# Kernel optimization log

Hardware: AMD Instinct MI355X
Metric: run time of the kernel (lower is better)

Reference implementation:

```python
import jax, jax.numpy as jnp
import numpy as np
from jax import lax

B = 4096
PRO_VOCAB, PRO_LEN, PRO_K = 25, 1000, 8
LIG_VOCAB, LIG_LEN, LIG_K = 64, 100, 4
CH = 96  # 2*CH = 192 = 6*32 per the reshape in the original forward
DN = ('NCH', 'OIH', 'NCH')  # 1D conv dimension numbers


def setup_inputs() -> dict:
    key = jax.random.key(0)
    ks = jax.random.split(key, 8)
    protein = jax.random.normal(ks[0], (B, PRO_VOCAB, PRO_LEN), dtype=jnp.float32)
    ligand = jax.random.normal(ks[1], (B, LIG_VOCAB, LIG_LEN), dtype=jnp.float32)
    w_pro = jax.random.normal(ks[2], (CH, PRO_VOCAB, PRO_K), dtype=jnp.float32) * 0.05
    b_pro = jnp.zeros((CH,), dtype=jnp.float32)
    w_lig = jax.random.normal(ks[3], (CH, LIG_VOCAB, LIG_K), dtype=jnp.float32) * 0.05
    b_lig = jnp.zeros((CH,), dtype=jnp.float32)
    # QuLinear readout over the 32*32=1024 amplitude-encoded Gram matrix -> scalar
    w_aff = jax.random.normal(ks[4], (1024,), dtype=jnp.float32) * 0.05
    b_aff = jnp.zeros((), dtype=jnp.float32)
    return {"protein": protein, "ligand": ligand, "w_pro": w_pro, "b_pro": b_pro,
            "w_lig": w_lig, "b_lig": b_lig, "w_aff": w_aff, "b_aff": b_aff}


def _conv_branch(x, w, b):
    # Conv1d (valid) -> ReLU -> global max pool over length  =>  (B, CH)
    y = lax.conv_general_dilated(x, w, (1,), 'VALID', dimension_numbers=DN)
    return jnp.max(jax.nn.relu(y + b[None, :, None]), axis=-1)


def reference(protein, ligand, w_pro, b_pro, w_lig, b_lig, w_aff, b_aff):
    x1 = _conv_branch(ligand, w_lig, b_lig)    # (B, 96)
    x2 = _conv_branch(protein, w_pro, b_pro)   # (B, 96)
    x = jnp.concatenate([x1, x2], axis=1).reshape(-1, 6, 32)  # (B, 6, 32)
    # Vectorized per-sample Gram matrix a.T @ a : (B, 32, 32)
    gram = jnp.einsum('bij,bik->bjk', x, x)
    flat = gram.reshape(gram.shape[0], -1)     # (B, 1024)
    # Amplitude encoding: L2-normalize the flattened Gram matrix per sample
    amp = flat / (jnp.linalg.norm(flat, axis=1, keepdims=True) + 1e-12)
    # QuLinear readout -> scalar affinity per sample
    aff = amp @ w_aff + b_aff                  # (B,)
    return aff
```

## Files before the change

kernel.cpp:

```cpp
#include <hip/hip_runtime.h>
#include <math.h>

typedef _Float16 f16;
typedef _Float16 f16x2 __attribute__((ext_vector_type(2)));
typedef _Float16 f16x4 __attribute__((ext_vector_type(4)));
typedef _Float16 f16x8 __attribute__((ext_vector_type(8)));
typedef float f32x4 __attribute__((ext_vector_type(4)));
typedef float f32x16 __attribute__((ext_vector_type(16)));

template<int V, int K, int VP>
__global__ void repack_kernel(const float* __restrict__ w, f16* __restrict__ wp) {
    int i = blockIdx.x * 256 + threadIdx.x;
    if (i >= K * 96 * VP) return;
    int v = i % VP, ch = (i / VP) % 96, t = i / (VP * 96);
    float val = (v < V) ? w[(ch * V + v) * K + t] : 0.f;
    wp[i] = (f16)val;
}

__global__ void repack_pro_kernel(const float* __restrict__ w, f16* __restrict__ wp) {
    constexpr int V = 25, K = 8;
    int i = blockIdx.x * 256 + threadIdx.x;
    if (i >= K * 6 * 64 * 8) return;
    int e = i & 7, l = (i >> 3) & 63, c6 = (i >> 9) % 6, t = i / (512 * 6);
    int r16 = l & 15, g = l >> 4;
    int ch = c6 * 16 + r16, v = g * 8 + e;
    float val = (v < V) ? w[(ch * V + v) * K + t] : 0.f;
    wp[i] = (f16)val;
}

__global__ __launch_bounds__(512, 4) void conv_pro_kernel(
    const float* __restrict__ in,
    const f16*   __restrict__ wp,
    const float* __restrict__ bias,
    float* __restrict__ feat,
    int feat_off)
{
    constexpr int V = 25, L = 1000, KT = 8, LOUT = 993;
    constexpr int CH  = 256;
    constexpr int NC  = 4;
    constexpr int BR  = 264;
    constexpr int RSB = 80;
    constexpr int P4  = BR / 4;
    constexpr int NVP = 13;
    constexpr int NU  = NVP * P4;
    constexpr int NW  = KT * 6 * 64 * 8;

    __shared__ __align__(16) char s_raw[BR * RSB];
    __shared__ __align__(16) f16  s_w[NW];
    __shared__ float s_red[8 * 96];

    const int tid  = threadIdx.x;
    const int wave = tid >> 6;
    const int lane = tid & 63;
    const int g    = lane >> 4;
    const int r16  = lane & 15;
    const size_t b = blockIdx.x;
    const float* gs = in + b * (size_t)(V * L);

    {
        const f16x8* wg = (const f16x8*)wp;
        f16x8* wl = (f16x8*)s_w;
        #pragma unroll
        for (int u = 0; u < NW / 8 / 512; ++u)
            wl[u * 512 + tid] = wg[u * 512 + tid];
    }
    for (int row = tid; row < BR; row += 512) {
        const int swz = ((row >> 3) & 3) << 4;
        *(f16x8*)(s_raw + row * RSB + (48 ^ swz)) = (f16x8){};
    }
    __syncthreads();

    float runmax[6];
    #pragma unroll
    for (int c6 = 0; c6 < 6; ++c6) runmax[c6] = -3.0e38f;

    for (int c = 0; c < NC; ++c) {
        if (c) __syncthreads();
        #pragma unroll
        for (int u = 0; u < 2; ++u) {
            const int i = u * 512 + tid;
            if (i < NU) {
                const int v2 = i / P4, p4 = i - v2 * P4;
                const int p  = 4 * p4;
                const int gp = c * CH + p;
                float4 x0 = {0.f, 0.f, 0.f, 0.f}, x1 = {0.f, 0.f, 0.f, 0.f};
                if (gp < L) {
                    x0 = *(const float4*)(gs + (size_t)(2 * v2) * L + gp);
                    if (2 * v2 + 1 < V)
                        x1 = *(const float4*)(gs + (size_t)(2 * v2 + 1) * L + gp);
                }
                const int pb = 4 * v2;
                const int slot = pb & 48, sub = pb & 12;
                const float vx0[4] = {x0.x, x0.y, x0.z, x0.w};
                const float vx1[4] = {x1.x, x1.y, x1.z, x1.w};
                #pragma unroll
                for (int j = 0; j < 4; ++j) {
                    const int row = p + j;
                    const int swz = ((row >> 3) & 3) << 4;
                    f16x2 hv = { (f16)vx0[j], (f16)vx1[j] };
                    *(f16x2*)(s_raw + row * RSB + ((slot ^ swz) + sub)) = hv;
                }
            }
        }
        __syncthreads();

        f32x4 acc[2][6] = {};
        #pragma unroll 1
        for (int t = 0; t < KT; ++t) {
            f16x8 bf[6];
            #pragma unroll
            for (int c6 = 0; c6 < 6; ++c6)
                bf[c6] = *(const f16x8*)(s_w + ((t * 6 + c6) * 64 + lane) * 8);
            #pragma unroll
            for (int rt = 0; rt < 2; ++rt) {
                const int row = wave * 32 + rt * 16 + r16 + t;
                const int swz = ((row >> 3) & 3) << 4;
                f16x8 a = *(const f16x8*)(s_raw + row * RSB + ((g * 16) ^ swz));
                #pragma unroll
                for (int c6 = 0; c6 < 6; ++c6)
                    acc[rt][c6] = __builtin_amdgcn_mfma_f32_16x16x32_f16(a, bf[c6], acc[rt][c6], 0, 0, 0);
            }
        }
        #pragma unroll
        for (int rt = 0; rt < 2; ++rt) {
            const int pt = c * CH + wave * 32 + rt * 16;
            if (pt + 16 <= LOUT) {
                #pragma unroll
                for (int c6 = 0; c6 < 6; ++c6)
                    #pragma unroll
                    for (int i = 0; i < 4; ++i)
                        runmax[c6] = fmaxf(runmax[c6], acc[rt][c6][i]);
            } else {
                const int p0g = pt + g * 4;
                #pragma unroll
                for (int c6 = 0; c6 < 6; ++c6)
                    #pragma unroll
                    for (int i = 0; i < 4; ++i)
                        if (p0g + i < LOUT) runmax[c6] = fmaxf(runmax[c6], acc[rt][c6][i]);
            }
        }
    }

    #pragma unroll
    for (int c6 = 0; c6 < 6; ++c6) {
        runmax[c6] = fmaxf(runmax[c6], __shfl_xor(runmax[c6], 16, 64));
        runmax[c6] = fmaxf(runmax[c6], __shfl_xor(runmax[c6], 32, 64));
    }
    if (lane < 16) {
        #pragma unroll
        for (int c6 = 0; c6 < 6; ++c6)
            s_red[wave * 96 + c6 * 16 + lane] = runmax[c6];
    }
    __syncthreads();
    if (tid < 96) {
        float m = s_red[tid];
        #pragma unroll
        for (int w = 1; w < 8; ++w) m = fmaxf(m, s_red[w * 96 + tid]);
        feat[b * 192 + feat_off + tid] = fmaxf(m + bias[tid], 0.f);
    }
}

__global__ __launch_bounds__(384) void conv_lig_kernel(
    const float* __restrict__ in,
    const f16*   __restrict__ wp,
    const float* __restrict__ bias,
    float* __restrict__ feat,
    int feat_off)
{
    constexpr int V = 64, L = 100, KT = 4, VP = 64, KSTEPS = 4;
    constexpr int LP = 132, RS = 72, NTILES = 4, LOUT = 97;
    constexpr int RSB = RS * 2, NQ = V / 4;
    __shared__ __align__(16) char s_raw[LP * RSB];

    const int tid  = threadIdx.x;
    const int b    = blockIdx.x;
    const int wave = tid >> 6;
    const int lane = tid & 63;
    const int colw = wave % 3;
    const int roww = wave / 3;
    const int q    = lane >> 5;
    const int r    = lane & 31;

    {
        float4 z = {0.f, 0.f, 0.f, 0.f};
        float4* sz = (float4*)s_raw;
        for (int i = tid; i < LP * RSB / 16; i += 384) sz[i] = z;
    }
    __syncthreads();

    const float* gin = in + (size_t)b * (V * L);
    for (int i = tid; i < NQ * L; i += 384) {
        int q4 = i / L, p = i - q4 * L;
        const float* gp = gin + q4 * 4 * L + p;
        f16x4 hv = { (f16)gp[0], (f16)gp[L], (f16)gp[2 * L], (f16)gp[3 * L] };
        int off = (8 * q4) ^ (((p >> 3) & 3) << 4);
        *(f16x4*)(s_raw + p * RSB + off) = hv;
    }

    f16x8 bfr[KT][KSTEPS];
    #pragma unroll
    for (int t = 0; t < KT; ++t)
        #pragma unroll
        for (int ks = 0; ks < KSTEPS; ++ks)
            bfr[t][ks] = *(const f16x8*)(wp + (t * 96 + colw * 32 + r) * VP + ks * 16 + q * 8);

    __syncthreads();

    float runmax = -3.0e38f;
    for (int it = 0; it < NTILES / 2; ++it) {
        const int p0 = (roww * (NTILES / 2) + it) * 32;
        f32x16 acc = {};
        #pragma unroll
        for (int t = 0; t < KT; ++t) {
            int row = p0 + r + t;
            if (row > LP - 1) row = LP - 1;
            const char* ap = s_raw + row * RSB;
            const int swz = ((row >> 3) & 3) << 4;
            #pragma unroll
            for (int ks = 0; ks < KSTEPS; ++ks) {
                f16x8 af = *(const f16x8*)(ap + ((ks * 32 + q * 16) ^ swz));
                acc = __builtin_amdgcn_mfma_f32_32x32x16_f16(af, bfr[t][ks], acc, 0, 0, 0);
            }
        }
        #pragma unroll
        for (int i = 0; i < 16; ++i) {
            int rr = (i & 3) + 8 * (i >> 2) + 4 * q;
            if (p0 + rr < LOUT) runmax = fmaxf(runmax, acc[i]);
        }
    }
    runmax = fmaxf(runmax, __shfl_xor(runmax, 32, 64));

    __syncthreads();
    float* s_red = (float*)s_raw;
    if (lane < 32) s_red[roww * 96 + colw * 32 + r] = runmax;
    __syncthreads();
    if (tid < 96) {
        float m = fmaxf(s_red[tid], s_red[96 + tid]);
        feat[(size_t)b * 192 + feat_off + tid] = fmaxf(m + bias[tid], 0.f);
    }
}

__global__ __launch_bounds__(256) void gram_affinity_kernel(
    const float* __restrict__ feat, const float* __restrict__ w_aff,
    const float* __restrict__ b_aff, float* __restrict__ out, int B)
{
    const int lane = threadIdx.x & 63;
    const int wid  = threadIdx.x >> 6;
    const int b    = blockIdx.x * 4 + wid;

    __shared__ float s_x[4][192];

    if (b < B) {
        const float* fp = feat + (size_t)b * 192;
        for (int i = lane; i < 192; i += 64) s_x[wid][i] = fp[i];
    }
    __syncthreads();

    if (b < B) {
        float ssum = 0.f, sdot = 0.f;
        #pragma unroll
        for (int t = 0; t < 16; ++t) {
            const int jk = t * 64 + lane;
            const int j = jk >> 5, k = jk & 31;
            float gg = 0.f;
            #pragma unroll
            for (int i = 0; i < 6; ++i)
                gg = fmaf(s_x[wid][i * 32 + j], s_x[wid][i * 32 + k], gg);
            ssum = fmaf(gg, gg, ssum);
            sdot = fmaf(gg, w_aff[jk], sdot);
        }
        #pragma unroll
        for (int off = 32; off >= 1; off >>= 1) {
            ssum += __shfl_xor(ssum, off, 64);
            sdot += __shfl_xor(sdot, off, 64);
        }
        if (lane == 0) out[b] = sdot / (sqrtf(ssum) + 1e-12f) + b_aff[0];
    }
}

extern "C" void kernel_launch(void* const* d_in, const int* in_sizes, int n_in,
                              void* d_out, int out_size, void* d_ws, size_t ws_size,
                              hipStream_t stream)
{
    const float* protein = (const float*)d_in[0];
    const float* ligand  = (const float*)d_in[1];
    const float* w_pro   = (const float*)d_in[2];
    const float* b_pro   = (const float*)d_in[3];
    const float* w_lig   = (const float*)d_in[4];
    const float* b_lig   = (const float*)d_in[5];
    const float* w_aff   = (const float*)d_in[6];
    const float* b_aff   = (const float*)d_in[7];
    float* out = (float*)d_out;
    const int B = out_size;

    float* feat   = (float*)d_ws;
    f16*   wpackP = (f16*)((char*)d_ws + (size_t)B * 192 * 4);
    f16*   wpackL = wpackP + 24576;

    repack_pro_kernel<<<96, 256, 0, stream>>>(w_pro, wpackP);
    repack_kernel<64, 4, 64><<<96, 256, 0, stream>>>(w_lig, wpackL);

    conv_lig_kernel<<<B, 384, 0, stream>>>(ligand, wpackL, b_lig, feat, 0);
    conv_pro_kernel<<<B, 512, 0, stream>>>(protein, wpackP, b_pro, feat, 96);

    gram_affinity_kernel<<<(B + 3) / 4, 256, 0, stream>>>(feat, w_aff, b_aff, out, B);
}
```

Before: 283.7 us.

## Merge ligand and protein conv into one launch with shared MFMA 16x16 path

Replaces the separate ligand and protein conv kernels with a single kernel launched over 2*B blocks. The first B blocks run the protein conv and the rest run the ligand conv. The ligand path is rewritten to use the same 16x16x32 MFMA tiling, with weights repacked and staged in LDS and seven waves each covering 16 output positions. The aim is to remove one launch and the tail of the smaller ligand kernel by letting both workloads share the GPU. In exchange, ligand blocks now reserve the protein kernel's large LDS footprint and 512 threads, which may lower their occupancy.

```diff
diff --git a/kernel.cpp b/kernel.cpp
--- a/kernel.cpp
+++ b/kernel.cpp
@@ -3,19 +3,8 @@
 
 typedef _Float16 f16;
 typedef _Float16 f16x2 __attribute__((ext_vector_type(2)));
-typedef _Float16 f16x4 __attribute__((ext_vector_type(4)));
 typedef _Float16 f16x8 __attribute__((ext_vector_type(8)));
 typedef float f32x4 __attribute__((ext_vector_type(4)));
-typedef float f32x16 __attribute__((ext_vector_type(16)));
-
-template<int V, int K, int VP>
-__global__ void repack_kernel(const float* __restrict__ w, f16* __restrict__ wp) {
-    int i = blockIdx.x * 256 + threadIdx.x;
-    if (i >= K * 96 * VP) return;
-    int v = i % VP, ch = (i / VP) % 96, t = i / (VP * 96);
-    float val = (v < V) ? w[(ch * V + v) * K + t] : 0.f;
-    wp[i] = (f16)val;
-}
 
 __global__ void repack_pro_kernel(const float* __restrict__ w, f16* __restrict__ wp) {
     constexpr int V = 25, K = 8;
@@ -28,25 +17,29 @@
     wp[i] = (f16)val;
 }
 
-__global__ __launch_bounds__(512, 4) void conv_pro_kernel(
-    const float* __restrict__ in,
-    const f16*   __restrict__ wp,
-    const float* __restrict__ bias,
+__global__ void repack_lig_kernel(const float* __restrict__ w, f16* __restrict__ wp) {
+    constexpr int V = 64, K = 4;
+    int i = blockIdx.x * 256 + threadIdx.x;
+    if (i >= 8 * 6 * 64 * 8) return;
+    int e = i & 7, l = (i >> 3) & 63, c6 = (i >> 9) % 6, tk = i / (512 * 6);
+    int t = tk >> 1, ks = tk & 1;
+    int r16 = l & 15, g = l >> 4;
+    int ch = c6 * 16 + r16, v = ks * 32 + g * 8 + e;
+    wp[i] = (f16)w[(ch * V + v) * K + t];
+}
+
+__global__ __launch_bounds__(512, 4) void conv_kernel(
+    const float* __restrict__ pro,
+    const f16*   __restrict__ wpP,
+    const float* __restrict__ bP,
+    const float* __restrict__ lig,
+    const f16*   __restrict__ wpL,
+    const float* __restrict__ bL,
     float* __restrict__ feat,
-    int feat_off)
+    int B)
 {
-    constexpr int V = 25, L = 1000, KT = 8, LOUT = 993;
-    constexpr int CH  = 256;
-    constexpr int NC  = 4;
-    constexpr int BR  = 264;
-    constexpr int RSB = 80;
-    constexpr int P4  = BR / 4;
-    constexpr int NVP = 13;
-    constexpr int NU  = NVP * P4;
-    constexpr int NW  = KT * 6 * 64 * 8;
-
-    __shared__ __align__(16) char s_raw[BR * RSB];
-    __shared__ __align__(16) f16  s_w[NW];
+    __shared__ __align__(16) char s_raw[264 * 80];
+    __shared__ __align__(16) f16  s_w[24576];
     __shared__ float s_red[8 * 96];
 
     const int tid  = threadIdx.x;
@@ -54,43 +47,140 @@
     const int lane = tid & 63;
     const int g    = lane >> 4;
     const int r16  = lane & 15;
-    const size_t b = blockIdx.x;
-    const float* gs = in + b * (size_t)(V * L);
-
-    {
-        const f16x8* wg = (const f16x8*)wp;
-        f16x8* wl = (f16x8*)s_w;
-        #pragma unroll
-        for (int u = 0; u < NW / 8 / 512; ++u)
-            wl[u * 512 + tid] = wg[u * 512 + tid];
-    }
-    for (int row = tid; row < BR; row += 512) {
-        const int swz = ((row >> 3) & 3) << 4;
-        *(f16x8*)(s_raw + row * RSB + (48 ^ swz)) = (f16x8){};
-    }
-    __syncthreads();
-
-    float runmax[6];
-    #pragma unroll
-    for (int c6 = 0; c6 < 6; ++c6) runmax[c6] = -3.0e38f;
-
-    for (int c = 0; c < NC; ++c) {
-        if (c) __syncthreads();
+
+    if ((int)blockIdx.x < B) {
+        constexpr int V = 25, L = 1000, KT = 8, LOUT = 993;
+        constexpr int CH = 256, NC = 4, BR = 264, RSB = 80;
+        constexpr int P4 = BR / 4, NVP = 13, NU = NVP * P4;
+        const size_t b = blockIdx.x;
+        const float* gs = pro + b * (size_t)(V * L);
+
+        {   const f16x8* wg = (const f16x8*)wpP;
+            f16x8* wl = (f16x8*)s_w;
+            #pragma unroll
+            for (int u = 0; u < 24576 / 8 / 512; ++u)
+                wl[u * 512 + tid] = wg[u * 512 + tid];
+        }
+        for (int row = tid; row < BR; row += 512) {
+            const int swz = ((row >> 3) & 3) << 4;
+            *(f16x8*)(s_raw + row * RSB + (48 ^ swz)) = (f16x8){};
+        }
+        __syncthreads();
+
+        float runmax[6];
+        #pragma unroll
+        for (int c6 = 0; c6 < 6; ++c6) runmax[c6] = -3.0e38f;
+
+        for (int c = 0; c < NC; ++c) {
+            if (c) __syncthreads();
+            #pragma unroll
+            for (int u = 0; u < 2; ++u) {
+                const int i = u * 512 + tid;
+                if (i < NU) {
+                    const int v2 = i / P4, p4 = i - v2 * P4;
+                    const int p  = 4 * p4;
+                    const int gp = c * CH + p;
+                    float4 x0 = {0.f, 0.f, 0.f, 0.f}, x1 = {0.f, 0.f, 0.f, 0.f};
+                    if (gp < L) {
+                        x0 = *(const float4*)(gs + (size_t)(2 * v2) * L + gp);
+                        if (2 * v2 + 1 < V)
+                            x1 = *(const float4*)(gs + (size_t)(2 * v2 + 1) * L + gp);
+                    }
+                    const int pb = 4 * v2;
+                    const int slot = pb & 48, sub = pb & 12;
+                    const float vx0[4] = {x0.x, x0.y, x0.z, x0.w};
+                    const float vx1[4] = {x1.x, x1.y, x1.z, x1.w};
+                    #pragma unroll
+                    for (int j = 0; j < 4; ++j) {
+                        const int row = p + j;
+                        const int swz = ((row >> 3) & 3) << 4;
+                        f16x2 hv = { (f16)vx0[j], (f16)vx1[j] };
+                        *(f16x2*)(s_raw + row * RSB + ((slot ^ swz) + sub)) = hv;
+                    }
+                }
+            }
+            __syncthreads();
+
+            f32x4 acc[2][6] = {};
+            #pragma unroll 1
+            for (int t = 0; t < KT; ++t) {
+                f16x8 bf[6];
+                #pragma unroll
+                for (int c6 = 0; c6 < 6; ++c6)
+                    bf[c6] = *(const f16x8*)(s_w + ((t * 6 + c6) * 64 + lane) * 8);
+                #pragma unroll
+                for (int rt = 0; rt < 2; ++rt) {
+                    const int row = wave * 32 + rt * 16 + r16 + t;
+                    const int swz = ((row >> 3) & 3) << 4;
+                    f16x8 a = *(const f16x8*)(s_raw + row * RSB + ((g * 16) ^ swz));
+                    #pragma unroll
+                    for (int c6 = 0; c6 < 6; ++c6)
+                        acc[rt][c6] = __builtin_amdgcn_mfma_f32_16x16x32_f16(a, bf[c6], acc[rt][c6], 0, 0, 0);
+                }
+            }
+            #pragma unroll
+            for (int rt = 0; rt < 2; ++rt) {
+                const int pt = c * CH + wave * 32 + rt * 16;
+                if (pt + 16 <= LOUT) {
+                    #pragma unroll
+                    for (int c6 = 0; c6 < 6; ++c6)
+                        #pragma unroll
+                        for (int i = 0; i < 4; ++i)
+                            runmax[c6] = fmaxf(runmax[c6], acc[rt][c6][i]);
+                } else {
+                    const int p0g = pt + g * 4;
+                    #pragma unroll
+                    for (int c6 = 0; c6 < 6; ++c6)
+                        #pragma unroll
+                        for (int i = 0; i < 4; ++i)
+                            if (p0g + i < LOUT) runmax[c6] = fmaxf(runmax[c6], acc[rt][c6][i]);
+                }
+            }
+        }
+
+        #pragma unroll
+        for (int c6 = 0; c6 < 6; ++c6) {
+            runmax[c6] = fmaxf(runmax[c6], __shfl_xor(runmax[c6], 16, 64));
+            runmax[c6] = fmaxf(runmax[c6], __shfl_xor(runmax[c6], 32, 64));
+        }
+        if (lane < 16) {
+            #pragma unroll
+            for (int c6 = 0; c6 < 6; ++c6)
+                s_red[wave * 96 + c6 * 16 + lane] = runmax[c6];
+        }
+        __syncthreads();
+        if (tid < 96) {
+            float m = s_red[tid];
+            #pragma unroll
+            for (int w = 1; w < 8; ++w) m = fmaxf(m, s_red[w * 96 + tid]);
+            feat[b * 192 + 96 + tid] = fmaxf(m + bP[tid], 0.f);
+        }
+    } else {
+        constexpr int V = 64, L = 100, KT = 4, LOUT = 97;
+        constexpr int BR = 120, RSB = 144;
+        constexpr int P4 = BR / 4, NVP = 32, NU = NVP * P4;
+        const size_t b = blockIdx.x - B;
+        const float* gs = lig + b * (size_t)(V * L);
+
+        {   const f16x8* wg = (const f16x8*)wpL;
+            f16x8* wl = (f16x8*)s_w;
+            #pragma unroll
+            for (int u = 0; u < 24576 / 8 / 512; ++u)
+                wl[u * 512 + tid] = wg[u * 512 + tid];
+        }
         #pragma unroll
         for (int u = 0; u < 2; ++u) {
             const int i = u * 512 + tid;
             if (i < NU) {
                 const int v2 = i / P4, p4 = i - v2 * P4;
                 const int p  = 4 * p4;
-                const int gp = c * CH + p;
                 float4 x0 = {0.f, 0.f, 0.f, 0.f}, x1 = {0.f, 0.f, 0.f, 0.f};
-                if (gp < L) {
-                    x0 = *(const float4*)(gs + (size_t)(2 * v2) * L + gp);
-                    if (2 * v2 + 1 < V)
-                        x1 = *(const float4*)(gs + (size_t)(2 * v2 + 1) * L + gp);
+                if (p < L) {
+                    x0 = *(const float4*)(gs + (size_t)(2 * v2) * L + p);
+                    x1 = *(const float4*)(gs + (size_t)(2 * v2 + 1) * L + p);
                 }
                 const int pb = 4 * v2;
-                const int slot = pb & 48, sub = pb & 12;
+                const int slot = pb & 0x70, sub = pb & 12;
                 const float vx0[4] = {x0.x, x0.y, x0.z, x0.w};
                 const float vx1[4] = {x1.x, x1.y, x1.z, x1.w};
                 #pragma unroll
@@ -104,139 +194,48 @@
         }
         __syncthreads();
 
-        f32x4 acc[2][6] = {};
-        #pragma unroll 1
-        for (int t = 0; t < KT; ++t) {
-            f16x8 bf[6];
-            #pragma unroll
-            for (int c6 = 0; c6 < 6; ++c6)
-                bf[c6] = *(const f16x8*)(s_w + ((t * 6 + c6) * 64 + lane) * 8);
-            #pragma unroll
-            for (int rt = 0; rt < 2; ++rt) {
-                const int row = wave * 32 + rt * 16 + r16 + t;
-                const int swz = ((row >> 3) & 3) << 4;
-                f16x8 a = *(const f16x8*)(s_raw + row * RSB + ((g * 16) ^ swz));
+        if (wave < 7) {
+            f32x4 acc[6] = {};
+            #pragma unroll 1
+            for (int t = 0; t < KT; ++t) {
+                #pragma unroll
+                for (int ks = 0; ks < 2; ++ks) {
+                    f16x8 bf[6];
+                    #pragma unroll
+                    for (int c6 = 0; c6 < 6; ++c6)
+                        bf[c6] = *(const f16x8*)(s_w + (((t * 2 + ks) * 6 + c6) * 64 + lane) * 8);
+                    const int row = wave * 16 + r16 + t;
+                    const int swz = ((row >> 3) & 3) << 4;
+                    f16x8 a = *(const f16x8*)(s_raw + row * RSB + ((ks * 64 + g * 16) ^ swz));
+                    #pragma unroll
+                    for (int c6 = 0; c6 < 6; ++c6)
+                        acc[c6] = __builtin_amdgcn_mfma_f32_16x16x32_f16(a, bf[c6], acc[c6], 0, 0, 0);
+                }
+            }
+            float runmax[6];
+            const int p0g = wave * 16 + g * 4;
+            #pragma unroll
+            for (int c6 = 0; c6 < 6; ++c6) {
+                runmax[c6] = -3.0e38f;
+                #pragma unroll
+                for (int i = 0; i < 4; ++i)
+                    if (p0g + i < LOUT) runmax[c6] = fmaxf(runmax[c6], acc[c6][i]);
+                runmax[c6] = fmaxf(runmax[c6], __shfl_xor(runmax[c6], 16, 64));
+                runmax[c6] = fmaxf(runmax[c6], __shfl_xor(runmax[c6], 32, 64));
+            }
+            if (lane < 16) {
                 #pragma unroll
                 for (int c6 = 0; c6 < 6; ++c6)
-                    acc[rt][c6] = __builtin_amdgcn_mfma_f32_16x16x32_f16(a, bf[c6], acc[rt][c6], 0, 0, 0);
-            }
-        }
-        #pragma unroll
-        for (int rt = 0; rt < 2; ++rt) {
-            const int pt = c * CH + wave * 32 + rt * 16;
-            if (pt + 16 <= LOUT) {
-                #pragma unroll
-                for (int c6 = 0; c6 < 6; ++c6)
-                    #pragma unroll
-                    for (int i = 0; i < 4; ++i)
-                        runmax[c6] = fmaxf(runmax[c6], acc[rt][c6][i]);
-            } else {
-                const int p0g = pt + g * 4;
-                #pragma unroll
-                for (int c6 = 0; c6 < 6; ++c6)
-                    #pragma unroll
-                    for (int i = 0; i < 4; ++i)
-                        if (p0g + i < LOUT) runmax[c6] = fmaxf(runmax[c6], acc[rt][c6][i]);
-            }
-        }
-    }
-
-    #pragma unroll
-    for (int c6 = 0; c6 < 6; ++c6) {
-        runmax[c6] = fmaxf(runmax[c6], __shfl_xor(runmax[c6], 16, 64));
-        runmax[c6] = fmaxf(runmax[c6], __shfl_xor(runmax[c6], 32, 64));
-    }
-    if (lane < 16) {
-        #pragma unroll
-        for (int c6 = 0; c6 < 6; ++c6)
-            s_red[wave * 96 + c6 * 16 + lane] = runmax[c6];
-    }
-    __syncthreads();
-    if (tid < 96) {
-        float m = s_red[tid];
-        #pragma unroll
-        for (int w = 1; w < 8; ++w) m = fmaxf(m, s_red[w * 96 + tid]);
-        feat[b * 192 + feat_off + tid] = fmaxf(m + bias[tid], 0.f);
-    }
-}
-
-__global__ __launch_bounds__(384) void conv_lig_kernel(
-    const float* __restrict__ in,
-    const f16*   __restrict__ wp,
-    const float* __restrict__ bias,
-    float* __restrict__ feat,
-    int feat_off)
-{
-    constexpr int V = 64, L = 100, KT = 4, VP = 64, KSTEPS = 4;
-    constexpr int LP = 132, RS = 72, NTILES = 4, LOUT = 97;
-    constexpr int RSB = RS * 2, NQ = V / 4;
-    __shared__ __align__(16) char s_raw[LP * RSB];
-
-    const int tid  = threadIdx.x;
-    const int b    = blockIdx.x;
-    const int wave = tid >> 6;
-    const int lane = tid & 63;
-    const int colw = wave % 3;
-    const int roww = wave / 3;
-    const int q    = lane >> 5;
-    const int r    = lane & 31;
-
-    {
-        float4 z = {0.f, 0.f, 0.f, 0.f};
-        float4* sz = (float4*)s_raw;
-        for (int i = tid; i < LP * RSB / 16; i += 384) sz[i] = z;
-    }
-    __syncthreads();
-
-    const float* gin = in + (size_t)b * (V * L);
-    for (int i = tid; i < NQ * L; i += 384) {
-        int q4 = i / L, p = i - q4 * L;
-        const float* gp = gin + q4 * 4 * L + p;
-        f16x4 hv = { (f16)gp[0], (f16)gp[L], (f16)gp[2 * L], (f16)gp[3 * L] };
-        int off = (8 * q4) ^ (((p >> 3) & 3) << 4);
-        *(f16x4*)(s_raw + p * RSB + off) = hv;
-    }
-
-    f16x8 bfr[KT][KSTEPS];
-    #pragma unroll
-    for (int t = 0; t < KT; ++t)
-        #pragma unroll
-        for (int ks = 0; ks < KSTEPS; ++ks)
-            bfr[t][ks] = *(const f16x8*)(wp + (t * 96 + colw * 32 + r) * VP + ks * 16 + q * 8);
-
-    __syncthreads();
-
-    float runmax = -3.0e38f;
-    for (int it = 0; it < NTILES / 2; ++it) {
-        const int p0 = (roww * (NTILES / 2) + it) * 32;
-        f32x16 acc = {};
-        #pragma unroll
-        for (int t = 0; t < KT; ++t) {
-            int row = p0 + r + t;
-            if (row > LP - 1) row = LP - 1;
-            const char* ap = s_raw + row * RSB;
-            const int swz = ((row >> 3) & 3) << 4;
-            #pragma unroll
-            for (int ks = 0; ks < KSTEPS; ++ks) {
-                f16x8 af = *(const f16x8*)(ap + ((ks * 32 + q * 16) ^ swz));
-                acc = __builtin_amdgcn_mfma_f32_32x32x16_f16(af, bfr[t][ks], acc, 0, 0, 0);
-            }
-        }
-        #pragma unroll
-        for (int i = 0; i < 16; ++i) {
-            int rr = (i & 3) + 8 * (i >> 2) + 4 * q;
-            if (p0 + rr < LOUT) runmax = fmaxf(runmax, acc[i]);
-        }
-    }
-    runmax = fmaxf(runmax, __shfl_xor(runmax, 32, 64));
-
-    __syncthreads();
-    float* s_red = (float*)s_raw;
-    if (lane < 32) s_red[roww * 96 + colw * 32 + r] = runmax;
-    __syncthreads();
-    if (tid < 96) {
-        float m = fmaxf(s_red[tid], s_red[96 + tid]);
-        feat[(size_t)b * 192 + feat_off + tid] = fmaxf(m + bias[tid], 0.f);
+                    s_red[wave * 96 + c6 * 16 + lane] = runmax[c6];
+            }
+        }
+        __syncthreads();
+        if (tid < 96) {
+            float m = s_red[tid];
+            #pragma unroll
+            for (int w = 1; w < 7; ++w) m = fmaxf(m, s_red[w * 96 + tid]);
+            feat[b * 192 + tid] = fmaxf(m + bL[tid], 0.f);
+        }
     }
 }
 
@@ -298,10 +297,10 @@
     f16*   wpackL = wpackP + 24576;
 
     repack_pro_kernel<<<96, 256, 0, stream>>>(w_pro, wpackP);
-    repack_kernel<64, 4, 64><<<96, 256, 0, stream>>>(w_lig, wpackL);
-
-    conv_lig_kernel<<<B, 384, 0, stream>>>(ligand, wpackL, b_lig, feat, 0);
-    conv_pro_kernel<<<B, 512, 0, stream>>>(protein, wpackP, b_pro, feat, 96);
+    repack_lig_kernel<<<96, 256, 0, stream>>>(w_lig, wpackL);
+
+    conv_kernel<<<2 * B, 512, 0, stream>>>(
+        protein, wpackP, b_pro, ligand, wpackL, b_lig, feat, B);
 
     gram_affinity_kernel<<<(B + 3) / 4, 256, 0, stream>>>(feat, w_aff, b_aff, out, B);
 }
```

New measurement: 249.4 us. -12.1%, faster.
